# Performance work log

Hardware: AMD Instinct MI355X
Metric: run time of the kernel (lower is better)

## Reference

```python
import jax, jax.numpy as jnp
import numpy as np

NUM_HEADS = 32
ROPE_BASE = 10000.0
VISION_TOKEN_TYPE = 1


def _rotate_half(x):
    x1, x2 = jnp.split(x, 2, axis=-1)
    return jnp.concatenate([-x2, x1], axis=-1)


def _rope_cos_sin(position_ids, head_dim, dtype):
    # position_ids: [L] int -> cos/sin [L, head_dim]
    inv_freq = 1.0 / (ROPE_BASE ** (jnp.arange(0, head_dim, 2, dtype=jnp.float32) / head_dim))
    freqs = position_ids.astype(jnp.float32)[:, None] * inv_freq[None, :]  # [L, head_dim//2]
    emb = jnp.concatenate([freqs, freqs], axis=-1)  # [L, head_dim]
    return jnp.cos(emb).astype(dtype), jnp.sin(emb).astype(dtype)


def setup_inputs() -> dict:
    key = jax.random.key(0)
    ks = jax.random.split(key, 7)
    B, L, D = 2, 1024, 4096
    w_scale = 0.02
    return {
        'hidden_states': jax.random.normal(ks[0], (B, L, D), dtype=jnp.float32),
        'token_type_ids': jax.random.randint(ks[1], (B, L), 0, 2, dtype=jnp.int32),
        'position_ids': jnp.arange(L, dtype=jnp.int64),
        'w_qkv_vis': jax.random.normal(ks[2], (D, 3 * D), dtype=jnp.float32) * w_scale,
        'w_qkv_lang': jax.random.normal(ks[3], (D, 3 * D), dtype=jnp.float32) * w_scale,
        'w_dense_vis': jax.random.normal(ks[4], (D, D), dtype=jnp.float32) * w_scale,
        'w_dense_lang': jax.random.normal(ks[5], (D, D), dtype=jnp.float32) * w_scale,
    }


def reference(hidden_states, token_type_ids, position_ids, w_qkv_vis, w_qkv_lang, w_dense_vis, w_dense_lang):
    B, L, D = hidden_states.shape
    H = NUM_HEADS
    Dh = D // H

    # expert masks: a token is 'vision' iff it and the NEXT token are vision type
    tt = token_type_ids
    vmask = jnp.zeros(tt.shape, dtype=bool)
    vmask = vmask.at[:, :-1].set((tt[:, :-1] == VISION_TOKEN_TYPE) & (tt[:, 1:] == VISION_TOKEN_TYPE))  # [B, L]

    # dual-expert fused QKV projection (mask-select between experts)
    qkv = jnp.where(vmask[..., None],
                    hidden_states @ w_qkv_vis,
                    hidden_states @ w_qkv_lang)  # [B, L, 3D]
    q, k, v = jnp.split(qkv, 3, axis=-1)
    q = q.reshape(B, L, H, Dh)
    k = k.reshape(B, L, H, Dh)
    v = v.reshape(B, L, H, Dh)

    # rotary embedding
    cos, sin = _rope_cos_sin(position_ids, Dh, q.dtype)  # [L, Dh]
    cos = cos[None, :, None, :]
    sin = sin[None, :, None, :]
    q = q * cos + _rotate_half(q) * sin
    k = k * cos + _rotate_half(k) * sin

    # causal self-attention (prefill semantics of paged_attention_fwd)
    scale = 1.0 / jnp.sqrt(jnp.asarray(Dh, dtype=q.dtype))
    scores = jnp.einsum('blhd,bmhd->bhlm', q, k) * scale  # [B, H, L, L]
    causal = jnp.tril(jnp.ones((L, L), dtype=bool))
    scores = jnp.where(causal[None, None], scores, jnp.asarray(-1e30, dtype=scores.dtype))
    probs = jax.nn.softmax(scores, axis=-1)
    ctx = jnp.einsum('bhlm,bmhd->blhd', probs, v).reshape(B, L, D)

    # dual-expert output projection
    attn_output = jnp.where(vmask[..., None],
                            ctx @ w_dense_vis,
                            ctx @ w_dense_lang)  # [B, L, D]
    return attn_output
```

## Files before the change

### kernel.cpp

```cpp
#include <hip/hip_runtime.h>
#include <math.h>

typedef unsigned short u16;
typedef __attribute__((ext_vector_type(4))) float f32x4;
typedef __attribute__((ext_vector_type(8))) __bf16 bf16x8;
typedef __attribute__((ext_vector_type(8))) u16 u16x8;
typedef __attribute__((ext_vector_type(4))) u16 u16x4;

#define D_MODEL 4096
#define NQKV    12288
#define BL      2048
#define L_SEQ   1024
#define NH      32
#define DH      128

__device__ __forceinline__ u16 f2bf(float f) {
    union { float f; unsigned u; } v; v.f = f;
    unsigned r = (v.u + 0x7fffu + ((v.u >> 16) & 1u)) >> 16;
    return (u16)r;
}
__device__ __forceinline__ float bf2f(u16 b) {
    union { unsigned u; float f; } v; v.u = ((unsigned)b) << 16;
    return v.f;
}
__device__ __forceinline__ void gload_lds16(const void* g, void* l) {
    __builtin_amdgcn_global_load_lds((const __attribute__((address_space(1))) void*)g,
                                     (__attribute__((address_space(3))) void*)l, 16, 0, 0);
}
__device__ __forceinline__ f32x4 mfma_bf16(bf16x8 a, bf16x8 b, f32x4 c) {
    return __builtin_amdgcn_mfma_f32_16x16x32_bf16(a, b, c, 0, 0, 0);
}

#define BAR()      asm volatile("s_barrier" ::: "memory")
#define WAIT_VM4() asm volatile("s_waitcnt vmcnt(4)" ::: "memory")
#define WAIT_VM0() asm volatile("s_waitcnt vmcnt(0)" ::: "memory")

__global__ __launch_bounds__(256) void convert_f32_bf16(const float* __restrict__ in,
                                                        u16* __restrict__ out, int n4) {
    int i = blockIdx.x * 256 + threadIdx.x;
    if (i < n4) {
        float4 v = ((const float4*)in)[i];
        u16x4 o;
        o[0] = f2bf(v.x); o[1] = f2bf(v.y); o[2] = f2bf(v.z); o[3] = f2bf(v.w);
        ((u16x4*)out)[i] = o;
    }
}

__global__ __launch_bounds__(256) void transpose_convert(const float* __restrict__ W,
                                                         u16* __restrict__ Wt, int K, int N) {
    __shared__ float t[32][33];
    int tx = threadIdx.x, ty = threadIdx.y;
    int nt = blockIdx.x * 32, kt = blockIdx.y * 32;
#pragma unroll
    for (int i = 0; i < 4; ++i)
        t[ty + i * 8][tx] = W[(size_t)(kt + ty + i * 8) * N + nt + tx];
    __syncthreads();
#pragma unroll
    for (int i = 0; i < 4; ++i)
        Wt[(size_t)(nt + ty + i * 8) * K + kt + tx] = f2bf(t[tx][ty + i * 8]);
}

__global__ __launch_bounds__(256) void mask_scan(const int* __restrict__ tt,
                                                 int* __restrict__ lists,
                                                 int* __restrict__ counts) {
    __shared__ int buf[256];
    int tid = threadIdx.x;
    int base = tid * 8;
    int flags = 0, cv = 0;
#pragma unroll
    for (int j = 0; j < 8; ++j) {
        int i = base + j;
        int l = i & (L_SEQ - 1);
        int f = (l < L_SEQ - 1) && (tt[i] == 1) && (tt[i + 1] == 1);
        flags |= f << j; cv += f;
    }
    buf[tid] = cv; __syncthreads();
    for (int d = 1; d < 256; d <<= 1) {
        int t = (tid >= d) ? buf[tid - d] : 0;
        __syncthreads();
        buf[tid] += t;
        __syncthreads();
    }
    int vs = buf[tid] - cv;
    int ls = base - vs;
    int total_v = buf[255];
#pragma unroll
    for (int j = 0; j < 8; ++j) {
        int i = base + j;
        if ((flags >> j) & 1) lists[vs++] = i;
        else                  lists[2048 + ls++] = i;
    }
    if (tid == 0) { counts[0] = total_v; counts[1] = 2048 - total_v; }
}

template <typename OutT>
__global__ __launch_bounds__(512, 2) void gemm_expert(
    const u16* __restrict__ A, const u16* __restrict__ BtVis, const u16* __restrict__ BtLang,
    OutT* __restrict__ C, const int* __restrict__ lists, const int* __restrict__ counts, int ldc) {
    const int e = blockIdx.z;
    const int cnt = counts[e];
    const int m0 = blockIdx.y * 256;
    if (m0 >= cnt) return;
    const u16* Bt = (e == 0) ? BtVis : BtLang;
    const int* list = lists + e * 2048;
    const int n0 = blockIdx.x * 256;
    const int tid = threadIdx.x, lane = tid & 63, w = tid >> 6;
    const int wm = w >> 2, wn = w & 3;
    const int l16 = lane & 15, quad = lane >> 4;

    __shared__ __align__(16) u16 lds[2][2][2][8192];

    const int r0 = tid >> 2;
    const int cs = (tid & 3) ^ ((r0 >> 1) & 3);
    const char* pa0 = (const char*)(A + (size_t)list[min(m0 + r0, cnt - 1)] * D_MODEL) + cs * 16;
    const char* pa1 = (const char*)(A + (size_t)list[min(m0 + 128 + r0, cnt - 1)] * D_MODEL) + cs * 16;
    const char* pb0 = (const char*)(Bt + (size_t)(n0 + r0) * D_MODEL) + cs * 16;
    const char* pb1 = (const char*)(Bt + (size_t)(n0 + 128 + r0) * D_MODEL) + cs * 16;
    const int dst0 = w * 512;
    const int dst1 = 4096 + w * 512;

    auto STAGE = [&](int buf, int mat, int kh, int tk) {
        const int kbyte = tk * 128 + kh * 64;
        const char* g0 = (mat == 0) ? pa0 : pb0;
        const char* g1 = (mat == 0) ? pa1 : pb1;
        u16* d = &lds[buf][mat][kh][0];
        gload_lds16(g0 + kbyte, d + dst0);
        gload_lds16(g1 + kbyte, d + dst1);
    };

    f32x4 acc[8][4] = {};
    const int NT = D_MODEL / 64;

    STAGE(0, 0, 0, 0); STAGE(0, 1, 0, 0); STAGE(0, 0, 1, 0); STAGE(0, 1, 1, 0);
    WAIT_VM4();
    BAR();

    for (int t = 0; t < NT; ++t) {
        const int c = t & 1, nb = c ^ 1;
        const bool pf = (t + 1 < NT);
        bf16x8 af[4], bf[4];

#pragma unroll
        for (int ni = 0; ni < 4; ++ni) {
            int row = wn * 64 + ni * 16 + l16;
            bf[ni] = *(const bf16x8*)&lds[c][1][0][row * 32 + (quad ^ ((row >> 1) & 3)) * 8];
        }
#pragma unroll
        for (int mi = 0; mi < 4; ++mi) {
            int row = wm * 128 + mi * 16 + l16;
            af[mi] = *(const bf16x8*)&lds[c][0][0][row * 32 + (quad ^ ((row >> 1) & 3)) * 8];
        }
        if (pf) STAGE(nb, 0, 0, t + 1);
        BAR();
        __builtin_amdgcn_s_setprio(1);
#pragma unroll
        for (int mi = 0; mi < 4; ++mi)
#pragma unroll
            for (int ni = 0; ni < 4; ++ni)
                acc[mi][ni] = mfma_bf16(af[mi], bf[ni], acc[mi][ni]);
        __builtin_amdgcn_s_setprio(0);
        BAR();

#pragma unroll
        for (int mi = 0; mi < 4; ++mi) {
            int row = wm * 128 + 64 + mi * 16 + l16;
            af[mi] = *(const bf16x8*)&lds[c][0][0][row * 32 + (quad ^ ((row >> 1) & 3)) * 8];
        }
        if (pf) STAGE(nb, 1, 0, t + 1);
        BAR();
        __builtin_amdgcn_s_setprio(1);
#pragma unroll
        for (int mi = 0; mi < 4; ++mi)
#pragma unroll
            for (int ni = 0; ni < 4; ++ni)
                acc[4 + mi][ni] = mfma_bf16(af[mi], bf[ni], acc[4 + mi][ni]);
        __builtin_amdgcn_s_setprio(0);
        if (pf) WAIT_VM4(); else WAIT_VM0();
        BAR();

#pragma unroll
        for (int ni = 0; ni < 4; ++ni) {
            int row = wn * 64 + ni * 16 + l16;
            bf[ni] = *(const bf16x8*)&lds[c][1][1][row * 32 + (quad ^ ((row >> 1) & 3)) * 8];
        }
#pragma unroll
        for (int mi = 0; mi < 4; ++mi) {
            int row = wm * 128 + mi * 16 + l16;
            af[mi] = *(const bf16x8*)&lds[c][0][1][row * 32 + (quad ^ ((row >> 1) & 3)) * 8];
        }
        if (pf) STAGE(nb, 0, 1, t + 1);
        BAR();
        __builtin_amdgcn_s_setprio(1);
#pragma unroll
        for (int mi = 0; mi < 4; ++mi)
#pragma unroll
            for (int ni = 0; ni < 4; ++ni)
                acc[mi][ni] = mfma_bf16(af[mi], bf[ni], acc[mi][ni]);
        __builtin_amdgcn_s_setprio(0);
        BAR();

#pragma unroll
        for (int mi = 0; mi < 4; ++mi) {
            int row = wm * 128 + 64 + mi * 16 + l16;
            af[mi] = *(const bf16x8*)&lds[c][0][1][row * 32 + (quad ^ ((row >> 1) & 3)) * 8];
        }
        if (pf) STAGE(nb, 1, 1, t + 1);
        BAR();
        __builtin_amdgcn_s_setprio(1);
#pragma unroll
        for (int mi = 0; mi < 4; ++mi)
#pragma unroll
            for (int ni = 0; ni < 4; ++ni)
                acc[4 + mi][ni] = mfma_bf16(af[mi], bf[ni], acc[4 + mi][ni]);
        __builtin_amdgcn_s_setprio(0);
        if (pf) WAIT_VM4();
        BAR();
    }

#pragma unroll
    for (int mf = 0; mf < 8; ++mf) {
#pragma unroll
        for (int r = 0; r < 4; ++r) {
            int slot = m0 + wm * 128 + mf * 16 + quad * 4 + r;
            if (slot < cnt) {
                int row = list[slot];
                size_t rb = (size_t)row * ldc + n0 + wn * 64 + l16;
#pragma unroll
                for (int ni = 0; ni < 4; ++ni) {
                    float v = acc[mf][ni][r];
                    if constexpr (sizeof(OutT) == 2) C[rb + ni * 16] = (OutT)f2bf(v);
                    else                             C[rb + ni * 16] = v;
                }
            }
        }
    }
}

__global__ __launch_bounds__(256) void rope_kernel(u16* __restrict__ qkv,
                                                   const int* __restrict__ posi) {
    int idx = blockIdx.x * 256 + threadIdx.x;
    int t = idx >> 11;
    int rem = idx & 2047;
    int h = rem >> 6;
    int j = rem & 63;
    int l = t & (L_SEQ - 1);
    int is_i32 = posi[1];
    int pv = is_i32 ? posi[l] : posi[2 * l];
    float p = (float)pv;
    float inv = expf(-(float)j * 0.14391156831212787f);
    float ang = p * inv;
    float s, c;
    sincosf(ang, &s, &c);
    size_t base = (size_t)t * NQKV + h * DH + j;
    float x1 = bf2f(qkv[base]), x2 = bf2f(qkv[base + 64]);
    qkv[base]      = f2bf(x1 * c - x2 * s);
    qkv[base + 64] = f2bf(x2 * c + x1 * s);
    size_t kb = base + D_MODEL;
    x1 = bf2f(qkv[kb]); x2 = bf2f(qkv[kb + 64]);
    qkv[kb]      = f2bf(x1 * c - x2 * s);
    qkv[kb + 64] = f2bf(x2 * c + x1 * s);
}

__global__ __launch_bounds__(256) void attn_kernel(const u16* __restrict__ qkv,
                                                   u16* __restrict__ ctx) {
    const int qt = blockIdx.x, h = blockIdx.y, b = blockIdx.z;
    const int tid = threadIdx.x, lane = tid & 63, w = tid >> 6;
    const int quad = lane >> 4, l16 = lane & 15;

    __shared__ __align__(16) u16 Qs[64 * 128];
    __shared__ __align__(16) u16 Ks[32 * 128];
    __shared__ __align__(16) u16 Vt[128 * 32];
    __shared__ __align__(16) u16 Ps[4][16 * 32];

    const size_t qbase = ((size_t)(b * L_SEQ + qt * 64)) * NQKV + h * DH;
    for (int idx = tid; idx < 64 * 16; idx += 256) {
        int r = idx >> 4, c = idx & 15;
        *(u16x8*)&Qs[r * 128 + c * 8] = *(const u16x8*)&qkv[qbase + (size_t)r * NQKV + c * 8];
    }

    float m_i[4], l_i[4];
    f32x4 o[8] = {};
#pragma unroll
    for (int r = 0; r < 4; ++r) { m_i[r] = -1e30f; l_i[r] = 0.f; }
    const float scale = 0.08838834764831845f;
    const int jmax = 2 * qt + 2;

    for (int jt = 0; jt < jmax; ++jt) {
        __syncthreads();
        const size_t kb = ((size_t)(b * L_SEQ + jt * 32)) * NQKV + D_MODEL + h * DH;
        const size_t vb = kb + D_MODEL;
        for (int idx = tid; idx < 32 * 16; idx += 256) {
            int r = idx >> 4, c = idx & 15;
            *(u16x8*)&Ks[r * 128 + c * 8] = *(const u16x8*)&qkv[kb + (size_t)r * NQKV + c * 8];
            u16x8 v = *(const u16x8*)&qkv[vb + (size_t)r * NQKV + c * 8];
#pragma unroll
            for (int jj = 0; jj < 8; ++jj) Vt[(c * 8 + jj) * 32 + r] = v[jj];
        }
        __syncthreads();

        f32x4 s0 = {0.f, 0.f, 0.f, 0.f}, s1 = {0.f, 0.f, 0.f, 0.f};
#pragma unroll
        for (int kc = 0; kc < 4; ++kc) {
            bf16x8 aq  = *(const bf16x8*)&Qs[(w * 16 + l16) * 128 + kc * 32 + quad * 8];
            bf16x8 bk0 = *(const bf16x8*)&Ks[l16 * 128 + kc * 32 + quad * 8];
            bf16x8 bk1 = *(const bf16x8*)&Ks[(16 + l16) * 128 + kc * 32 + quad * 8];
            s0 = mfma_bf16(aq, bk0, s0);
            s1 = mfma_bf16(aq, bk1, s1);
        }

        const int qg = qt * 64 + w * 16 + quad * 4;
        const int kg0 = jt * 32 + l16, kg1 = kg0 + 16;
        float sv0[4], sv1[4], mx[4];
#pragma unroll
        for (int r = 0; r < 4; ++r) {
            sv0[r] = (kg0 <= qg + r) ? s0[r] * scale : -1e30f;
            sv1[r] = (kg1 <= qg + r) ? s1[r] * scale : -1e30f;
            mx[r] = fmaxf(sv0[r], sv1[r]);
        }
#pragma unroll
        for (int d = 1; d < 16; d <<= 1)
#pragma unroll
            for (int r = 0; r < 4; ++r) mx[r] = fmaxf(mx[r], __shfl_xor(mx[r], d));
        float alpha[4], p0[4], p1[4], rs[4];
#pragma unroll
        for (int r = 0; r < 4; ++r) {
            float mn = fmaxf(m_i[r], mx[r]);
            alpha[r] = __expf(m_i[r] - mn);
            m_i[r] = mn;
            p0[r] = __expf(sv0[r] - mn);
            p1[r] = __expf(sv1[r] - mn);
            rs[r] = p0[r] + p1[r];
        }
#pragma unroll
        for (int d = 1; d < 16; d <<= 1)
#pragma unroll
            for (int r = 0; r < 4; ++r) rs[r] += __shfl_xor(rs[r], d);
#pragma unroll
        for (int r = 0; r < 4; ++r) {
            l_i[r] = l_i[r] * alpha[r] + rs[r];
            Ps[w][(quad * 4 + r) * 32 + l16]      = f2bf(p0[r]);
            Ps[w][(quad * 4 + r) * 32 + 16 + l16] = f2bf(p1[r]);
        }
#pragma unroll
        for (int n = 0; n < 8; ++n)
#pragma unroll
            for (int r = 0; r < 4; ++r) o[n][r] *= alpha[r];
        __syncthreads();
        bf16x8 ap = *(const bf16x8*)&Ps[w][l16 * 32 + quad * 8];
#pragma unroll
        for (int n = 0; n < 8; ++n) {
            bf16x8 bv = *(const bf16x8*)&Vt[(n * 16 + l16) * 32 + quad * 8];
            o[n] = mfma_bf16(ap, bv, o[n]);
        }
    }

    const int tglob = b * L_SEQ + qt * 64 + w * 16 + quad * 4;
#pragma unroll
    for (int r = 0; r < 4; ++r) {
        float invl = 1.f / l_i[r];
#pragma unroll
        for (int n = 0; n < 8; ++n)
            ctx[(size_t)(tglob + r) * D_MODEL + h * DH + n * 16 + l16] = f2bf(o[n][r] * invl);
    }
}

extern "C" void kernel_launch(void* const* d_in, const int* in_sizes, int n_in,
                              void* d_out, int out_size, void* d_ws, size_t ws_size,
                              hipStream_t stream) {
    const float* hidden = (const float*)d_in[0];
    const int* tt = (const int*)d_in[1];
    const int* pos = (const int*)d_in[2];
    const float* wqv = (const float*)d_in[3];
    const float* wql = (const float*)d_in[4];
    const float* wdv = (const float*)d_in[5];
    const float* wdl = (const float*)d_in[6];
    float* out = (float*)d_out;

    char* ws = (char*)d_ws;
    size_t off = 0;
    auto alloc = [&](size_t bytes) {
        char* p = ws + off;
        off += (bytes + 255) & ~(size_t)255;
        return p;
    };
    u16* WqvT = (u16*)alloc((size_t)NQKV * D_MODEL * 2);
    u16* WqlT = (u16*)alloc((size_t)NQKV * D_MODEL * 2);
    u16* WdvT = (u16*)alloc((size_t)D_MODEL * D_MODEL * 2);
    u16* WdlT = (u16*)alloc((size_t)D_MODEL * D_MODEL * 2);
    u16* Abf  = (u16*)alloc((size_t)BL * D_MODEL * 2);
    u16* QKV  = (u16*)alloc((size_t)BL * NQKV * 2);
    u16* CTX  = (u16*)alloc((size_t)BL * D_MODEL * 2);
    int* lists  = (int*)alloc(4096 * sizeof(int));
    int* counts = (int*)alloc(256);

    convert_f32_bf16<<<BL * D_MODEL / 4 / 256, 256, 0, stream>>>(hidden, Abf, BL * D_MODEL / 4);
    transpose_convert<<<dim3(NQKV / 32, D_MODEL / 32), dim3(32, 8), 0, stream>>>(wqv, WqvT, D_MODEL, NQKV);
    transpose_convert<<<dim3(NQKV / 32, D_MODEL / 32), dim3(32, 8), 0, stream>>>(wql, WqlT, D_MODEL, NQKV);
    transpose_convert<<<dim3(D_MODEL / 32, D_MODEL / 32), dim3(32, 8), 0, stream>>>(wdv, WdvT, D_MODEL, D_MODEL);
    transpose_convert<<<dim3(D_MODEL / 32, D_MODEL / 32), dim3(32, 8), 0, stream>>>(wdl, WdlT, D_MODEL, D_MODEL);
    mask_scan<<<1, 256, 0, stream>>>(tt, lists, counts);
    gemm_expert<u16><<<dim3(NQKV / 256, 8, 2), 512, 0, stream>>>(Abf, WqvT, WqlT, QKV, lists, counts, NQKV);
    rope_kernel<<<BL * NH * 64 / 256, 256, 0, stream>>>(QKV, pos);
    attn_kernel<<<dim3(16, NH, 2), 256, 0, stream>>>(QKV, CTX);
    gemm_expert<float><<<dim3(D_MODEL / 256, 8, 2), 512, 0, stream>>>(CTX, WdvT, WdlT, out, lists, counts, D_MODEL);
}
```

Before: 1.205 ms.

## Double-buffer 64-wide KV tiles with swizzled LDS and register-resident Q in attention

Reworks the attention kernel to process 64-key tiles instead of 32, keeping Q fragments in registers instead of shared memory. The next K/V tile is prefetched into registers and written to a second LDS buffer after compute, which overlaps global loads with MFMA work and drops to one barrier per tile. K, V-transpose and P tiles use XOR-swizzled layouts to avoid bank conflicts, blocks are launched heaviest-first, and setprio hints plus launch_bounds(256,2) are added. Costs are higher register and LDS usage, which may limit occupancy.

```diff
diff --git a/kernel.cpp b/kernel.cpp
--- a/kernel.cpp
+++ b/kernel.cpp
@@ -261,97 +261,170 @@
     qkv[kb + 64] = f2bf(x2 * c + x1 * s);
 }
 
-__global__ __launch_bounds__(256) void attn_kernel(const u16* __restrict__ qkv,
-                                                   u16* __restrict__ ctx) {
-    const int qt = blockIdx.x, h = blockIdx.y, b = blockIdx.z;
+__global__ __launch_bounds__(256, 2) void attn_kernel(const u16* __restrict__ qkv,
+                                                      u16* __restrict__ ctx) {
+    const int qt = (int)gridDim.x - 1 - (int)blockIdx.x;
+    const int h = blockIdx.y, b = blockIdx.z;
     const int tid = threadIdx.x, lane = tid & 63, w = tid >> 6;
     const int quad = lane >> 4, l16 = lane & 15;
 
-    __shared__ __align__(16) u16 Qs[64 * 128];
-    __shared__ __align__(16) u16 Ks[32 * 128];
-    __shared__ __align__(16) u16 Vt[128 * 32];
-    __shared__ __align__(16) u16 Ps[4][16 * 32];
-
-    const size_t qbase = ((size_t)(b * L_SEQ + qt * 64)) * NQKV + h * DH;
-    for (int idx = tid; idx < 64 * 16; idx += 256) {
-        int r = idx >> 4, c = idx & 15;
-        *(u16x8*)&Qs[r * 128 + c * 8] = *(const u16x8*)&qkv[qbase + (size_t)r * NQKV + c * 8];
-    }
+    __shared__ __align__(16) u16 Ks[2][64 * 128];
+    __shared__ __align__(16) u16 Vt[2][128 * 64];
+    __shared__ __align__(16) u16 Ps[4][16 * 64];
+
+    const size_t qbase = ((size_t)(b * L_SEQ + qt * 64 + w * 16 + l16)) * NQKV + h * DH;
+    bf16x8 aq[4];
+#pragma unroll
+    for (int kc = 0; kc < 4; ++kc)
+        aq[kc] = *(const bf16x8*)&qkv[qbase + kc * 32 + quad * 8];
+
+    int srow[4], schk[4];
+#pragma unroll
+    for (int i = 0; i < 4; ++i) {
+        int idx = i * 256 + tid;
+        srow[i] = idx >> 4;
+        schk[i] = idx & 15;
+    }
+    const size_t kv0 = ((size_t)(b * L_SEQ)) * NQKV + D_MODEL + h * DH;
 
     float m_i[4], l_i[4];
     f32x4 o[8] = {};
 #pragma unroll
     for (int r = 0; r < 4; ++r) { m_i[r] = -1e30f; l_i[r] = 0.f; }
     const float scale = 0.08838834764831845f;
-    const int jmax = 2 * qt + 2;
+    const int jmax = qt + 1;
+
+    {
+        u16x8 kr[4], vr[4];
+#pragma unroll
+        for (int i = 0; i < 4; ++i) {
+            size_t g = kv0 + (size_t)srow[i] * NQKV + schk[i] * 8;
+            kr[i] = *(const u16x8*)&qkv[g];
+            vr[i] = *(const u16x8*)&qkv[g + D_MODEL];
+        }
+#pragma unroll
+        for (int i = 0; i < 4; ++i) {
+            int r = srow[i], c = schk[i];
+            *(u16x8*)&Ks[0][r * 128 + ((c ^ (r & 7)) * 8)] = kr[i];
+#pragma unroll
+            for (int e = 0; e < 8; ++e) {
+                int d = c * 8 + e;
+                int sw = (r >> 3) ^ ((d ^ (d >> 3)) & 7);
+                Vt[0][d * 64 + sw * 8 + (r & 7)] = vr[i][e];
+            }
+        }
+    }
+    __syncthreads();
 
     for (int jt = 0; jt < jmax; ++jt) {
-        __syncthreads();
-        const size_t kb = ((size_t)(b * L_SEQ + jt * 32)) * NQKV + D_MODEL + h * DH;
-        const size_t vb = kb + D_MODEL;
-        for (int idx = tid; idx < 32 * 16; idx += 256) {
-            int r = idx >> 4, c = idx & 15;
-            *(u16x8*)&Ks[r * 128 + c * 8] = *(const u16x8*)&qkv[kb + (size_t)r * NQKV + c * 8];
-            u16x8 v = *(const u16x8*)&qkv[vb + (size_t)r * NQKV + c * 8];
-#pragma unroll
-            for (int jj = 0; jj < 8; ++jj) Vt[(c * 8 + jj) * 32 + r] = v[jj];
-        }
-        __syncthreads();
-
-        f32x4 s0 = {0.f, 0.f, 0.f, 0.f}, s1 = {0.f, 0.f, 0.f, 0.f};
-#pragma unroll
-        for (int kc = 0; kc < 4; ++kc) {
-            bf16x8 aq  = *(const bf16x8*)&Qs[(w * 16 + l16) * 128 + kc * 32 + quad * 8];
-            bf16x8 bk0 = *(const bf16x8*)&Ks[l16 * 128 + kc * 32 + quad * 8];
-            bf16x8 bk1 = *(const bf16x8*)&Ks[(16 + l16) * 128 + kc * 32 + quad * 8];
-            s0 = mfma_bf16(aq, bk0, s0);
-            s1 = mfma_bf16(aq, bk1, s1);
-        }
+        const int cur = jt & 1;
+        const bool pf = (jt + 1 < jmax);
+
+        u16x8 kr[4], vr[4];
+        if (pf) {
+            const size_t kb = kv0 + (size_t)((jt + 1) * 64) * NQKV;
+#pragma unroll
+            for (int i = 0; i < 4; ++i) {
+                size_t g = kb + (size_t)srow[i] * NQKV + schk[i] * 8;
+                kr[i] = *(const u16x8*)&qkv[g];
+                vr[i] = *(const u16x8*)&qkv[g + D_MODEL];
+            }
+        }
+
+        f32x4 s[4] = {};
+        __builtin_amdgcn_s_setprio(1);
+#pragma unroll
+        for (int sub = 0; sub < 4; ++sub) {
+            const int row = sub * 16 + l16;
+#pragma unroll
+            for (int kc = 0; kc < 4; ++kc) {
+                bf16x8 bk = *(const bf16x8*)&Ks[cur][row * 128 + (((kc * 4 + quad) ^ (row & 7)) * 8)];
+                s[sub] = mfma_bf16(aq[kc], bk, s[sub]);
+            }
+        }
+        __builtin_amdgcn_s_setprio(0);
 
         const int qg = qt * 64 + w * 16 + quad * 4;
-        const int kg0 = jt * 32 + l16, kg1 = kg0 + 16;
-        float sv0[4], sv1[4], mx[4];
-#pragma unroll
-        for (int r = 0; r < 4; ++r) {
-            sv0[r] = (kg0 <= qg + r) ? s0[r] * scale : -1e30f;
-            sv1[r] = (kg1 <= qg + r) ? s1[r] * scale : -1e30f;
-            mx[r] = fmaxf(sv0[r], sv1[r]);
+        float p[4][4], mx[4];
+#pragma unroll
+        for (int r = 0; r < 4; ++r) mx[r] = -1e30f;
+#pragma unroll
+        for (int sub = 0; sub < 4; ++sub) {
+            const int kg = jt * 64 + sub * 16 + l16;
+#pragma unroll
+            for (int r = 0; r < 4; ++r) {
+                float sv = (kg <= qg + r) ? s[sub][r] * scale : -1e30f;
+                p[sub][r] = sv;
+                mx[r] = fmaxf(mx[r], sv);
+            }
         }
 #pragma unroll
         for (int d = 1; d < 16; d <<= 1)
 #pragma unroll
             for (int r = 0; r < 4; ++r) mx[r] = fmaxf(mx[r], __shfl_xor(mx[r], d));
-        float alpha[4], p0[4], p1[4], rs[4];
+        float alpha[4], rs[4];
 #pragma unroll
         for (int r = 0; r < 4; ++r) {
             float mn = fmaxf(m_i[r], mx[r]);
             alpha[r] = __expf(m_i[r] - mn);
             m_i[r] = mn;
-            p0[r] = __expf(sv0[r] - mn);
-            p1[r] = __expf(sv1[r] - mn);
-            rs[r] = p0[r] + p1[r];
-        }
+            rs[r] = 0.f;
+        }
+#pragma unroll
+        for (int sub = 0; sub < 4; ++sub)
+#pragma unroll
+            for (int r = 0; r < 4; ++r) {
+                p[sub][r] = __expf(p[sub][r] - m_i[r]);
+                rs[r] += p[sub][r];
+            }
 #pragma unroll
         for (int d = 1; d < 16; d <<= 1)
 #pragma unroll
             for (int r = 0; r < 4; ++r) rs[r] += __shfl_xor(rs[r], d);
-#pragma unroll
-        for (int r = 0; r < 4; ++r) {
-            l_i[r] = l_i[r] * alpha[r] + rs[r];
-            Ps[w][(quad * 4 + r) * 32 + l16]      = f2bf(p0[r]);
-            Ps[w][(quad * 4 + r) * 32 + 16 + l16] = f2bf(p1[r]);
-        }
+
+#pragma unroll
+        for (int sub = 0; sub < 4; ++sub)
+#pragma unroll
+            for (int r = 0; r < 4; ++r) {
+                const int q = quad * 4 + r;
+                const int chunk = sub * 2 + (l16 >> 3);
+                Ps[w][q * 64 + ((chunk ^ (q & 7)) * 8) + (l16 & 7)] = f2bf(p[sub][r]);
+            }
+#pragma unroll
+        for (int r = 0; r < 4; ++r) l_i[r] = l_i[r] * alpha[r] + rs[r];
 #pragma unroll
         for (int n = 0; n < 8; ++n)
 #pragma unroll
             for (int r = 0; r < 4; ++r) o[n][r] *= alpha[r];
+
+        __builtin_amdgcn_s_setprio(1);
+#pragma unroll
+        for (int ks = 0; ks < 2; ++ks) {
+            bf16x8 ap = *(const bf16x8*)&Ps[w][l16 * 64 + (((ks * 4 + quad) ^ (l16 & 7)) * 8)];
+#pragma unroll
+            for (int n = 0; n < 8; ++n) {
+                const int d = n * 16 + l16;
+                bf16x8 bv = *(const bf16x8*)&Vt[cur][d * 64 + (((ks * 4 + quad) ^ ((d ^ (d >> 3)) & 7)) * 8)];
+                o[n] = mfma_bf16(ap, bv, o[n]);
+            }
+        }
+        __builtin_amdgcn_s_setprio(0);
+
+        if (pf) {
+            const int nb = cur ^ 1;
+#pragma unroll
+            for (int i = 0; i < 4; ++i) {
+                int r = srow[i], c = schk[i];
+                *(u16x8*)&Ks[nb][r * 128 + ((c ^ (r & 7)) * 8)] = kr[i];
+#pragma unroll
+                for (int e = 0; e < 8; ++e) {
+                    int d = c * 8 + e;
+                    int sw = (r >> 3) ^ ((d ^ (d >> 3)) & 7);
+                    Vt[nb][d * 64 + sw * 8 + (r & 7)] = vr[i][e];
+                }
+            }
+        }
         __syncthreads();
-        bf16x8 ap = *(const bf16x8*)&Ps[w][l16 * 32 + quad * 8];
-#pragma unroll
-        for (int n = 0; n < 8; ++n) {
-            bf16x8 bv = *(const bf16x8*)&Vt[(n * 16 + l16) * 32 + quad * 8];
-            o[n] = mfma_bf16(ap, bv, o[n]);
-        }
     }
 
     const int tglob = b * L_SEQ + qt * 64 + w * 16 + quad * 4;
```

Result: faster. 1.025 ms (-14.9%).
